# Performance work log

Measured on AMD Instinct MI355X. Metric: run time of the kernel, lower is better.

Reference implementation:

```python
import jax, jax.numpy as jnp
import numpy as np

TEMPERATURE = 0.07
IGNORE_LABEL = -1
EPS = 1e-8


def setup_inputs() -> dict:
    key = jax.random.key(0)
    k1, k2, k3 = jax.random.split(key, 3)
    N = 100000
    E = 6400000
    edge_index = jax.random.randint(k1, (2, E), 0, N, dtype=jnp.int64)
    edge_logits = jax.random.normal(k2, (E,), dtype=jnp.float32)
    label = jax.random.randint(k3, (N,), 0, 20, dtype=jnp.int64)
    return {"edge_index": edge_index, "edge_logits": edge_logits, "label": label}


def reference(edge_index, edge_logits, label):
    N = label.shape[0]
    idx_i = edge_index[0]
    idx_j = edge_index[1]
    label_i = label[idx_i]
    label_j = label[idx_j]
    valid = (label_i != IGNORE_LABEL) & (label_j != IGNORE_LABEL)
    is_pos = (label_i == label_j) & valid
    is_neg = (label_i != label_j) & valid

    # node is a boundary node if it has at least one valid negative edge
    neg_count = jax.ops.segment_sum(is_neg.astype(jnp.float32), idx_i, num_segments=N)
    is_boundary = (neg_count > 0) & (label != IGNORE_LABEL)

    # edges whose source node is a boundary node (torch filters invalid edges first)
    edge_is_boundary = is_boundary[idx_i] & valid
    exp_logits = jnp.exp(edge_logits / TEMPERATURE)
    w = jnp.where(edge_is_boundary, exp_logits, 0.0)

    denominator = jax.ops.segment_sum(w, idx_i, num_segments=N)
    numerator = jax.ops.segment_sum(jnp.where(is_pos, w, 0.0), idx_i, num_segments=N)

    valid_boundary = is_boundary & (denominator > 0)
    per_node = jnp.where(
        valid_boundary,
        jnp.log(denominator + EPS) - jnp.log(numerator + EPS),
        0.0,
    )
    count = jnp.maximum(jnp.sum(valid_boundary.astype(jnp.float32)), 1.0)
    return jnp.sum(per_node) / count
```

## Files before the change

### kernel.cpp

```cpp
#include <hip/hip_runtime.h>
#include <hip/hip_fp16.h>

#define INV_T  (1.0f / 0.07f)
#define EPS    1e-8f

#define RSH     11
#define RNODES  (1 << RSH)
#define GSPLIT  32
#define SBLK    256
#define EPT     8
#define EPB     (SBLK * EPT)
#define MAXB    256
#define LINV    31u

__global__ void cbl_pack_lab5(const int* __restrict__ label,
                              unsigned char* __restrict__ lab5, int N) {
    int i = blockIdx.x * blockDim.x + threadIdx.x;
    if (i < N) {
        int v = label[i];
        lab5[i] = (v >= 0 && v < 31) ? (unsigned char)v : (unsigned char)LINV;
    }
}

__global__ __launch_bounds__(SBLK) void cbl_scatter(
    const int* __restrict__ idx_i,
    const int* __restrict__ idx_j,
    const float* __restrict__ logits,
    const unsigned char* __restrict__ lab5,
    unsigned* __restrict__ table_t,
    unsigned* __restrict__ payload,
    int E, int B, int nBlkPad) {
    __shared__ unsigned s_cnt[4][MAXB];
    __shared__ unsigned s_wb[4][MAXB];
    __shared__ unsigned s_tot[MAXB];
    __shared__ unsigned s_pref[MAXB];
    __shared__ __align__(16) unsigned s_stage[EPB];

    const int wave = threadIdx.x >> 6;
    const int lane = threadIdx.x & 63;

    for (int t = threadIdx.x; t < B; t += SBLK) {
        s_cnt[0][t] = 0; s_cnt[1][t] = 0; s_cnt[2][t] = 0; s_cnt[3][t] = 0;
    }
    __syncthreads();

    const int blockStart = blockIdx.x * EPB;
    int      barr[EPT];
    unsigned marr[EPT];

#pragma unroll
    for (int q = 0; q < EPT / 4; ++q) {
        int base = blockStart + (q * SBLK + threadIdx.x) * 4;
        if (base < E) {
            int4   ii = *reinterpret_cast<const int4*>(idx_i + base);
            int4   jj = *reinterpret_cast<const int4*>(idx_j + base);
            float4 lg = *reinterpret_cast<const float4*>(logits + base);
            int iv[4] = {ii.x, ii.y, ii.z, ii.w};
            int jv[4] = {jj.x, jj.y, jj.z, jj.w};
            float lv[4] = {lg.x, lg.y, lg.z, lg.w};
#pragma unroll
            for (int r = 0; r < 4; ++r) {
                unsigned lj = lab5[jv[r]];
                unsigned hb = (lj != LINV)
                    ? (unsigned)__half_as_ushort(__float2half(lv[r] * INV_T))
                    : 0xFC00u;
                marr[q * 4 + r] = (hb << 16) | (lj << 11)
                                | ((unsigned)iv[r] & (RNODES - 1));
                int b = (iv[r] >> RSH) & (MAXB - 1);
                barr[q * 4 + r] = b;
                atomicAdd(&s_cnt[wave][b], 1u);
            }
        } else {
#pragma unroll
            for (int r = 0; r < 4; ++r) barr[q * 4 + r] = -1;
        }
    }
    __syncthreads();

    for (int t = threadIdx.x; t < B; t += SBLK)
        s_tot[t] = s_cnt[0][t] + s_cnt[1][t] + s_cnt[2][t] + s_cnt[3][t];
    __syncthreads();

    if (B <= 64) {
        if (threadIdx.x < 64) {
            unsigned v = (lane < B) ? s_tot[lane] : 0u;
            unsigned incl = v;
            for (int off = 1; off < 64; off <<= 1) {
                unsigned n = __shfl_up(incl, off, 64);
                if (lane >= off) incl += n;
            }
            if (lane < B) s_pref[lane] = incl - v;
        }
    } else {
        if (threadIdx.x == 0) {
            unsigned r = 0;
            for (int b = 0; b < B; ++b) { s_pref[b] = r; r += s_tot[b]; }
        }
    }
    __syncthreads();

    for (int t = threadIdx.x; t < B; t += SBLK) {
        unsigned pref = s_pref[t];
        table_t[(size_t)t * nBlkPad + blockIdx.x] = (pref << 16) | s_tot[t];
        unsigned gb = pref;
        s_wb[0][t] = gb;  gb += s_cnt[0][t];
        s_wb[1][t] = gb;  gb += s_cnt[1][t];
        s_wb[2][t] = gb;  gb += s_cnt[2][t];
        s_wb[3][t] = gb;
        s_cnt[0][t] = 0; s_cnt[1][t] = 0; s_cnt[2][t] = 0; s_cnt[3][t] = 0;
    }
    __syncthreads();

#pragma unroll
    for (int k = 0; k < EPT; ++k) {
        int b = barr[k];
        if (b < 0) continue;
        unsigned slot = s_wb[wave][b] + atomicAdd(&s_cnt[wave][b], 1u);
        s_stage[slot] = marr[k];
    }
    __syncthreads();

    int lim = E - blockStart; if (lim > EPB) lim = EPB;
    int lim4 = lim >> 2;
    const uint4* src4 = reinterpret_cast<const uint4*>(s_stage);
    uint4* dst4 = reinterpret_cast<uint4*>(payload + blockStart);
    for (int t = threadIdx.x; t < lim4; t += SBLK) dst4[t] = src4[t];
}

__global__ __launch_bounds__(256) void cbl_accum(
    const unsigned* __restrict__ payload,
    const unsigned* __restrict__ table_t,
    const unsigned char* __restrict__ lab5,
    float* __restrict__ partials,
    int N, int B, int nBlkPad) {
    int b = blockIdx.x / GSPLIT;
    int g = blockIdx.x % GSPLIT;

    __shared__ float         acc[RNODES * 2];
    __shared__ unsigned char slab[RNODES];

    for (int t = threadIdx.x; t < RNODES * 2; t += 256) acc[t] = 0.0f;
    int nodeBase = b << RSH;
    for (int t = threadIdx.x; t < RNODES; t += 256) {
        int n = nodeBase + t;
        slab[t] = (n < N) ? lab5[n] : (unsigned char)LINV;
    }
    __syncthreads();

    int wave = threadIdx.x >> 6, lane = threadIdx.x & 63;
    int ngroups = nBlkPad >> 2;
    const unsigned* trow = table_t + (size_t)b * nBlkPad;

    for (int gg = g * 4 + wave; gg < ngroups; gg += GSPLIT * 4) {
        unsigned c0 = (unsigned)gg * 4u;
        uint4 t4 = *reinterpret_cast<const uint4*>(trow + c0);
        unsigned cnt0 = t4.x & 0xFFFFu, cnt1 = t4.y & 0xFFFFu;
        unsigned cnt2 = t4.z & 0xFFFFu, cnt3 = t4.w & 0xFFFFu;
        unsigned s0 = c0 * EPB + (t4.x >> 16);
        unsigned s1 = (c0 + 1) * EPB + (t4.y >> 16);
        unsigned s2 = (c0 + 2) * EPB + (t4.z >> 16);
        unsigned s3 = (c0 + 3) * EPB + (t4.w >> 16);
        unsigned p1 = cnt0, p2 = p1 + cnt1, p3 = p2 + cnt2;
        unsigned total = p3 + cnt3;
        for (unsigned k = lane; k < total; k += 64) {
            unsigned addr = (k < p1) ? (s0 + k)
                          : (k < p2) ? (s1 + (k - p1))
                          : (k < p3) ? (s2 + (k - p2))
                          :            (s3 + (k - p3));
            unsigned p = payload[addr];
            unsigned local = p & (RNODES - 1);
            unsigned lj    = (p >> 11) & 31u;
            unsigned li    = slab[local];
            float x = __half2float(__ushort_as_half((unsigned short)(p >> 16)));
            float w = (li == LINV) ? 0.0f : __expf(x);
            atomicAdd(&acc[(local << 1) | (li == lj ? 1u : 0u)], w);
        }
    }
    __syncthreads();

    float* dst = partials + (size_t)blockIdx.x * (RNODES * 2);
    for (int t = threadIdx.x; t < RNODES * 2; t += 256) dst[t] = acc[t];
}

__global__ __launch_bounds__(256) void cbl_loss(
    const float* __restrict__ partials,
    float* __restrict__ acc2, int N) {
    float lsum = 0.0f, lcnt = 0.0f;
    int stride = gridDim.x * blockDim.x;
    for (int n = blockIdx.x * blockDim.x + threadIdx.x; n < N; n += stride) {
        int b = n >> RSH;
        int local = n & (RNODES - 1);
        float neg = 0.0f, pos = 0.0f;
#pragma unroll 4
        for (int g = 0; g < GSPLIT; ++g) {
            const float* p = partials
                + (size_t)(b * GSPLIT + g) * (RNODES * 2) + local * 2;
            float2 v = *reinterpret_cast<const float2*>(p);
            neg += v.x;
            pos += v.y;
        }
        if (neg > 0.0f) {
            lsum += logf(neg + pos + EPS) - logf(pos + EPS);
            lcnt += 1.0f;
        }
    }
    for (int off = 32; off > 0; off >>= 1) {
        lsum += __shfl_down(lsum, off, 64);
        lcnt += __shfl_down(lcnt, off, 64);
    }
    __shared__ float s_sum[4];
    __shared__ float s_cnt2[4];
    int wid = threadIdx.x >> 6, lane = threadIdx.x & 63;
    if (lane == 0) { s_sum[wid] = lsum; s_cnt2[wid] = lcnt; }
    __syncthreads();
    if (threadIdx.x == 0) {
        float bs = 0.0f, bc = 0.0f;
        for (int w = 0; w < 4; ++w) { bs += s_sum[w]; bc += s_cnt2[w]; }
        atomicAdd(&acc2[0], bs);
        atomicAdd(&acc2[1], bc);
    }
}

__global__ void cbl_finalize(const float* __restrict__ acc2,
                             float* __restrict__ out) {
    out[0] = acc2[0] / fmaxf(acc2[1], 1.0f);
}

__global__ __launch_bounds__(256) void cbl_edge_fb(
    const int* __restrict__ idx_i, const int* __restrict__ idx_j,
    const float* __restrict__ logits, const unsigned char* __restrict__ lab5,
    float* __restrict__ buf, int E) {
    int stride = gridDim.x * blockDim.x;
    for (int e = blockIdx.x * blockDim.x + threadIdx.x; e < E; e += stride) {
        unsigned li = lab5[idx_i[e]];
        unsigned lj = lab5[idx_j[e]];
        if (li == LINV || lj == LINV) continue;
        float w = __expf(logits[e] * INV_T);
        int slot = (idx_i[e] << 1) | (li == lj ? 1 : 0);
        atomicAdd(&buf[slot], w);
    }
}

__global__ __launch_bounds__(256) void cbl_loss_fb(
    const float* __restrict__ buf, float* __restrict__ acc2, int N) {
    float lsum = 0.0f, lcnt = 0.0f;
    int stride = gridDim.x * blockDim.x;
    for (int n = blockIdx.x * blockDim.x + threadIdx.x; n < N; n += stride) {
        float neg = buf[2 * n], pos = buf[2 * n + 1];
        if (neg > 0.0f) {
            lsum += logf(neg + pos + EPS) - logf(pos + EPS);
            lcnt += 1.0f;
        }
    }
    for (int off = 32; off > 0; off >>= 1) {
        lsum += __shfl_down(lsum, off, 64);
        lcnt += __shfl_down(lcnt, off, 64);
    }
    __shared__ float s_sum[4];
    __shared__ float s_cnt2[4];
    int wid = threadIdx.x >> 6, lane = threadIdx.x & 63;
    if (lane == 0) { s_sum[wid] = lsum; s_cnt2[wid] = lcnt; }
    __syncthreads();
    if (threadIdx.x == 0) {
        float bs = 0.0f, bc = 0.0f;
        for (int w = 0; w < 4; ++w) { bs += s_sum[w]; bc += s_cnt2[w]; }
        atomicAdd(&acc2[0], bs);
        atomicAdd(&acc2[1], bc);
    }
}

extern "C" void kernel_launch(void* const* d_in, const int* in_sizes, int n_in,
                              void* d_out, int out_size, void* d_ws, size_t ws_size,
                              hipStream_t stream) {
    const int*   edge_index = (const int*)d_in[0];
    const float* logits     = (const float*)d_in[1];
    const int*   label      = (const int*)d_in[2];

    const int E = in_sizes[1];
    const int N = in_sizes[2];
    const int* idx_i = edge_index;
    const int* idx_j = edge_index + E;

    const int B       = (N + RNODES - 1) >> RSH;
    const int nBlk    = (E + EPB - 1) / EPB;
    const int nBlkPad = (nBlk + 3) & ~3;
    const int block   = 256;

    char* p = (char*)d_ws;
    float*    acc2   = (float*)p;               p += 16;
    unsigned char* lab5 = (unsigned char*)p;    p += ((size_t)N + 15) & ~(size_t)15;
    unsigned* table_t = (unsigned*)p;           p += (((size_t)B * nBlkPad * 4) + 15) & ~(size_t)15;
    unsigned* payload = (unsigned*)p;           p += (((size_t)E * 4) + 15) & ~(size_t)15;
    float*    partials = (float*)p;             p += (size_t)B * GSPLIT * RNODES * 2 * 4;
    size_t need = (size_t)(p - (char*)d_ws);

    const bool fast = (ws_size >= need) && ((E & 3) == 0) && (E >= 4) &&
                      (B >= 1) && (B <= MAXB) &&
                      (((uintptr_t)payload & 15) == 0) &&
                      (((uintptr_t)table_t & 15) == 0);

    if (fast) {
        hipMemsetAsync(acc2, 0, 8, stream);
        cbl_pack_lab5<<<(N + block - 1) / block, block, 0, stream>>>(label, lab5, N);

        cbl_scatter<<<nBlkPad, SBLK, 0, stream>>>(idx_i, idx_j, logits, lab5,
                                                  table_t, payload, E, B, nBlkPad);

        cbl_accum<<<B * GSPLIT, block, 0, stream>>>(payload, table_t, lab5,
                                                    partials, N, B, nBlkPad);

        int g5 = (N + block - 1) / block; if (g5 > 1024) g5 = 1024;
        cbl_loss<<<g5, block, 0, stream>>>(partials, acc2, N);
        cbl_finalize<<<1, 1, 0, stream>>>(acc2, (float*)d_out);
    } else {
        float* buf = (float*)d_ws;
        float* facc = buf + (size_t)2 * N;
        unsigned char* flab = (unsigned char*)(facc + 2);
        hipMemsetAsync(d_ws, 0, (size_t)N * 8 + 8, stream);
        cbl_pack_lab5<<<(N + block - 1) / block, block, 0, stream>>>(label, flab, N);
        int ge = (E + block - 1) / block; if (ge > 8192) ge = 8192;
        cbl_edge_fb<<<ge, block, 0, stream>>>(idx_i, idx_j, logits, flab, buf, E);
        int g5 = (N + block - 1) / block; if (g5 > 1024) g5 = 1024;
        cbl_loss_fb<<<g5, block, 0, stream>>>(buf, facc, N);
        cbl_finalize<<<1, 1, 0, stream>>>(facc, (float*)d_out);
    }
}
```

Before: 107.2 us.

## Halve node buckets, batch eight scatter blocks per wave, unroll accum loads

Node buckets shrink from 2048 to 1024 nodes. That doubles the bucket count and the accumulation grid while halving the shared accumulator per block. The scatter kernel's bucket-offset scan is rewritten as a two-wave shuffle scan covering up to 128 buckets, and the fast path is restricted to that limit. The accumulation kernel now reads eight table entries per group and issues two payload loads per loop iteration to raise memory-level parallelism, and its shared zeroing and output copy use float4. In exchange it adds address-select work per element and more per-block bucket counters in scatter.

```diff
diff --git a/kernel.cpp b/kernel.cpp
--- a/kernel.cpp
+++ b/kernel.cpp
@@ -4,7 +4,7 @@
 #define INV_T  (1.0f / 0.07f)
 #define EPS    1e-8f
 
-#define RSH     11
+#define RSH     10
 #define RNODES  (1 << RSH)
 #define GSPLIT  32
 #define SBLK    256
@@ -77,26 +77,23 @@
     }
     __syncthreads();
 
-    for (int t = threadIdx.x; t < B; t += SBLK)
-        s_tot[t] = s_cnt[0][t] + s_cnt[1][t] + s_cnt[2][t] + s_cnt[3][t];
-    __syncthreads();
-
-    if (B <= 64) {
-        if (threadIdx.x < 64) {
-            unsigned v = (lane < B) ? s_tot[lane] : 0u;
-            unsigned incl = v;
-            for (int off = 1; off < 64; off <<= 1) {
-                unsigned n = __shfl_up(incl, off, 64);
-                if (lane >= off) incl += n;
-            }
-            if (lane < B) s_pref[lane] = incl - v;
-        }
-    } else {
-        if (threadIdx.x == 0) {
-            unsigned r = 0;
-            for (int b = 0; b < B; ++b) { s_pref[b] = r; r += s_tot[b]; }
-        }
-    }
+    for (int t = threadIdx.x; t < 128; t += SBLK)
+        s_tot[t] = (t < B)
+            ? s_cnt[0][t] + s_cnt[1][t] + s_cnt[2][t] + s_cnt[3][t] : 0u;
+    __syncthreads();
+
+    if (threadIdx.x < 128) {
+        unsigned v = s_tot[threadIdx.x];
+        unsigned incl = v;
+        for (int off = 1; off < 64; off <<= 1) {
+            unsigned n = __shfl_up(incl, off, 64);
+            if (lane >= off) incl += n;
+        }
+        s_pref[threadIdx.x] = incl - v;
+    }
+    __syncthreads();
+    if (threadIdx.x >= 64 && threadIdx.x < 128)
+        s_pref[threadIdx.x] += s_pref[63] + s_tot[63];
     __syncthreads();
 
     for (int t = threadIdx.x; t < B; t += SBLK) {
@@ -136,10 +133,12 @@
     int b = blockIdx.x / GSPLIT;
     int g = blockIdx.x % GSPLIT;
 
-    __shared__ float         acc[RNODES * 2];
+    __shared__ __align__(16) float acc[RNODES * 2];
     __shared__ unsigned char slab[RNODES];
 
-    for (int t = threadIdx.x; t < RNODES * 2; t += 256) acc[t] = 0.0f;
+    float4* acc4 = reinterpret_cast<float4*>(acc);
+    for (int t = threadIdx.x; t < RNODES / 2; t += 256)
+        acc4[t] = make_float4(0.f, 0.f, 0.f, 0.f);
     int nodeBase = b << RSH;
     for (int t = threadIdx.x; t < RNODES; t += 256) {
         int n = nodeBase + t;
@@ -148,38 +147,68 @@
     __syncthreads();
 
     int wave = threadIdx.x >> 6, lane = threadIdx.x & 63;
-    int ngroups = nBlkPad >> 2;
+    int ngroups = nBlkPad >> 3;
     const unsigned* trow = table_t + (size_t)b * nBlkPad;
 
     for (int gg = g * 4 + wave; gg < ngroups; gg += GSPLIT * 4) {
-        unsigned c0 = (unsigned)gg * 4u;
-        uint4 t4 = *reinterpret_cast<const uint4*>(trow + c0);
-        unsigned cnt0 = t4.x & 0xFFFFu, cnt1 = t4.y & 0xFFFFu;
-        unsigned cnt2 = t4.z & 0xFFFFu, cnt3 = t4.w & 0xFFFFu;
-        unsigned s0 = c0 * EPB + (t4.x >> 16);
-        unsigned s1 = (c0 + 1) * EPB + (t4.y >> 16);
-        unsigned s2 = (c0 + 2) * EPB + (t4.z >> 16);
-        unsigned s3 = (c0 + 3) * EPB + (t4.w >> 16);
-        unsigned p1 = cnt0, p2 = p1 + cnt1, p3 = p2 + cnt2;
-        unsigned total = p3 + cnt3;
-        for (unsigned k = lane; k < total; k += 64) {
-            unsigned addr = (k < p1) ? (s0 + k)
-                          : (k < p2) ? (s1 + (k - p1))
-                          : (k < p3) ? (s2 + (k - p2))
-                          :            (s3 + (k - p3));
-            unsigned p = payload[addr];
-            unsigned local = p & (RNODES - 1);
-            unsigned lj    = (p >> 11) & 31u;
-            unsigned li    = slab[local];
-            float x = __half2float(__ushort_as_half((unsigned short)(p >> 16)));
-            float w = (li == LINV) ? 0.0f : __expf(x);
-            atomicAdd(&acc[(local << 1) | (li == lj ? 1u : 0u)], w);
-        }
-    }
-    __syncthreads();
-
-    float* dst = partials + (size_t)blockIdx.x * (RNODES * 2);
-    for (int t = threadIdx.x; t < RNODES * 2; t += 256) dst[t] = acc[t];
+        unsigned c0 = (unsigned)gg * 8u;
+        uint4 ta = *reinterpret_cast<const uint4*>(trow + c0);
+        uint4 tb = *reinterpret_cast<const uint4*>(trow + c0 + 4);
+        unsigned st0 = (c0 + 0) * EPB + (ta.x >> 16), cn0 = ta.x & 0xFFFFu;
+        unsigned st1 = (c0 + 1) * EPB + (ta.y >> 16), cn1 = ta.y & 0xFFFFu;
+        unsigned st2 = (c0 + 2) * EPB + (ta.z >> 16), cn2 = ta.z & 0xFFFFu;
+        unsigned st3 = (c0 + 3) * EPB + (ta.w >> 16), cn3 = ta.w & 0xFFFFu;
+        unsigned st4 = (c0 + 4) * EPB + (tb.x >> 16), cn4 = tb.x & 0xFFFFu;
+        unsigned st5 = (c0 + 5) * EPB + (tb.y >> 16), cn5 = tb.y & 0xFFFFu;
+        unsigned st6 = (c0 + 6) * EPB + (tb.z >> 16), cn6 = tb.z & 0xFFFFu;
+        unsigned st7 = (c0 + 7) * EPB + (tb.w >> 16), cn7 = tb.w & 0xFFFFu;
+        unsigned o1 = cn0, o2 = o1 + cn1, o3 = o2 + cn2, o4 = o3 + cn3;
+        unsigned o5 = o4 + cn4, o6 = o5 + cn5, o7 = o6 + cn6;
+        unsigned total = o7 + cn7;
+
+#define CBL_ADDR(k, out)                                   \
+        {   unsigned a_ = st0 + (k);                        \
+            a_ = ((k) >= o1) ? st1 + ((k) - o1) : a_;       \
+            a_ = ((k) >= o2) ? st2 + ((k) - o2) : a_;       \
+            a_ = ((k) >= o3) ? st3 + ((k) - o3) : a_;       \
+            a_ = ((k) >= o4) ? st4 + ((k) - o4) : a_;       \
+            a_ = ((k) >= o5) ? st5 + ((k) - o5) : a_;       \
+            a_ = ((k) >= o6) ? st6 + ((k) - o6) : a_;       \
+            a_ = ((k) >= o7) ? st7 + ((k) - o7) : a_;       \
+            out = a_; }
+
+        for (unsigned k = lane; k < total; k += 128) {
+            unsigned kb = k + 64;
+            bool hasb = (kb < total);
+            unsigned a1, a2;
+            CBL_ADDR(k, a1);
+            CBL_ADDR(hasb ? kb : k, a2);
+            unsigned p1 = payload[a1];
+            unsigned p2 = payload[a2];
+            {
+                unsigned local = p1 & (RNODES - 1);
+                unsigned lj    = (p1 >> 11) & 31u;
+                unsigned li    = slab[local];
+                float x = __half2float(__ushort_as_half((unsigned short)(p1 >> 16)));
+                float w = (li == LINV) ? 0.0f : __expf(x);
+                atomicAdd(&acc[(local << 1) | (li == lj ? 1u : 0u)], w);
+            }
+            if (hasb) {
+                unsigned local = p2 & (RNODES - 1);
+                unsigned lj    = (p2 >> 11) & 31u;
+                unsigned li    = slab[local];
+                float x = __half2float(__ushort_as_half((unsigned short)(p2 >> 16)));
+                float w = (li == LINV) ? 0.0f : __expf(x);
+                atomicAdd(&acc[(local << 1) | (li == lj ? 1u : 0u)], w);
+            }
+        }
+#undef CBL_ADDR
+    }
+    __syncthreads();
+
+    float4* dst4 = reinterpret_cast<float4*>(
+        partials + (size_t)blockIdx.x * (RNODES * 2));
+    for (int t = threadIdx.x; t < RNODES / 2; t += 256) dst4[t] = acc4[t];
 }
 
 __global__ __launch_bounds__(256) void cbl_loss(
@@ -283,7 +312,7 @@
 
     const int B       = (N + RNODES - 1) >> RSH;
     const int nBlk    = (E + EPB - 1) / EPB;
-    const int nBlkPad = (nBlk + 3) & ~3;
+    const int nBlkPad = (nBlk + 7) & ~7;
     const int block   = 256;
 
     char* p = (char*)d_ws;
@@ -295,9 +324,10 @@
     size_t need = (size_t)(p - (char*)d_ws);
 
     const bool fast = (ws_size >= need) && ((E & 3) == 0) && (E >= 4) &&
-                      (B >= 1) && (B <= MAXB) &&
+                      (B >= 1) && (B <= 128) &&
                       (((uintptr_t)payload & 15) == 0) &&
-                      (((uintptr_t)table_t & 15) == 0);
+                      (((uintptr_t)table_t & 15) == 0) &&
+                      (((uintptr_t)partials & 15) == 0);
 
     if (fast) {
         hipMemsetAsync(acc2, 0, 8, stream);
```

After: 109.7 us. +2.3%, slower.
